# Kernel optimization log

Measured on AMD Instinct MI355X. Metric: run time of the kernel, lower is better.

The kernel has to match this reference:

```python
import jax, jax.numpy as jnp
import numpy as np

N_HEADS = 12


def setup_inputs() -> dict:
    key = jax.random.key(0)
    ks = jax.random.split(key, 5)
    B, T, D = 4, 2048, 768
    std = 1.0 / np.sqrt(D)
    return {
        "x": jax.random.normal(ks[0], (B, T, D), jnp.float32),
        "W_qkv": jax.random.normal(ks[1], (3 * D, D), jnp.float32) * std,
        "b_qkv": jax.random.normal(ks[2], (3 * D,), jnp.float32) * 0.02,
        "W_proj": jax.random.normal(ks[3], (D, D), jnp.float32) * std,
        "b_proj": jax.random.normal(ks[4], (D,), jnp.float32) * 0.02,
    }


def reference(x, W_qkv, b_qkv, W_proj, b_proj):
    # x: [B, T, D]; intended 3D path of the module (dropout = eval-mode identity)
    B, T, D = x.shape
    H = N_HEADS
    Dh = D // H
    scale = Dh ** -0.5
    qkv = x @ W_qkv.T + b_qkv                       # [B, T, 3D]
    qkv = qkv.reshape(B, T, 3, H, Dh)
    q = jnp.transpose(qkv[:, :, 0], (0, 2, 1, 3))    # [B, H, T, Dh]
    k = jnp.transpose(qkv[:, :, 1], (0, 2, 1, 3))
    v = jnp.transpose(qkv[:, :, 2], (0, 2, 1, 3))
    attn = jnp.einsum("bhqd,bhkd->bhqk", q, k) * scale  # [B, H, T, T]
    scores = jax.nn.softmax(attn, axis=-1)
    out = jnp.einsum("bhqk,bhkd->bhqd", scores, v)       # [B, H, T, Dh]
    out = jnp.transpose(out, (0, 2, 1, 3)).reshape(B, T, D)
    return out @ W_proj.T + b_proj
```

## Files before the change

kernel.cpp:

```cpp
#include <hip/hip_runtime.h>
#include <hip/hip_bf16.h>
#include <stdint.h>

typedef __bf16 bf16;
typedef __bf16 bf16x8 __attribute__((ext_vector_type(8)));
typedef __bf16 bf16x4 __attribute__((ext_vector_type(4)));
typedef short  s16x4  __attribute__((ext_vector_type(4)));
typedef short  s16x8  __attribute__((ext_vector_type(8)));
typedef float  f32x4  __attribute__((ext_vector_type(4)));

#define N_B 4
#define N_T 2048
#define N_D 768
#define N_H 12
#define N_DH 64
#define M_TOT (N_B * N_T)

__device__ __forceinline__ void async_copy16(const bf16* g, bf16* l) {
    __builtin_amdgcn_global_load_lds(
        (const __attribute__((address_space(1))) unsigned int*)g,
        (__attribute__((address_space(3))) unsigned int*)l,
        16, 0, 0);
}

__launch_bounds__(256)
__global__ void f2bf3(const float* __restrict__ a, bf16* __restrict__ oa, int na,
                      const float* __restrict__ b, bf16* __restrict__ ob, int nb,
                      const float* __restrict__ c, bf16* __restrict__ oc) {
    int i = (blockIdx.x * 256 + threadIdx.x) * 4;
    const float* src; bf16* dst;
    if (i < na)            { src = a; dst = oa; }
    else if (i < na + nb)  { src = b; dst = ob; i -= na; }
    else                   { src = c; dst = oc; i -= na + nb; }
    const float4 v = *(const float4*)(src + i);
    dst[i]     = (bf16)v.x;
    dst[i + 1] = (bf16)v.y;
    dst[i + 2] = (bf16)v.z;
    dst[i + 3] = (bf16)v.w;
}

#define GEMM_CORE(A_PTR, B_PTR, KDIM)                                          \
    __shared__ bf16 lsA[128 * 32];                                             \
    __shared__ bf16 lsB[128 * 32];                                             \
    const int m0 = blockIdx.x * 128;                                           \
    const int n0 = blockIdx.y * 128;                                           \
    const int t  = threadIdx.x;                                                \
    const int w  = t >> 6, l = t & 63;                                         \
    const int wm = w & 1, wn = w >> 1;                                         \
    const int lr = l & 15, lq = l >> 4;                                        \
    f32x4 acc[4][4] = {};                                                      \
    const bf16* Ab = (A_PTR) + (size_t)(m0 + (t >> 2)) * (KDIM) + (t & 3) * 8; \
    const bf16* Bb = (B_PTR) + (size_t)(n0 + (t >> 2)) * (KDIM) + (t & 3) * 8; \
    bf16* lA = lsA + t * 8;                                                    \
    bf16* lB = lsB + t * 8;                                                    \
    for (int k0 = 0; k0 < (KDIM); k0 += 32) {                                  \
        __syncthreads();                                                       \
        async_copy16(Ab + k0, lA);                                             \
        async_copy16(Ab + (size_t)64 * (KDIM) + k0, lA + 2048);                \
        async_copy16(Bb + k0, lB);                                             \
        async_copy16(Bb + (size_t)64 * (KDIM) + k0, lB + 2048);                \
        __syncthreads();                                                       \
        bf16x8 af[4], bfr[4];                                                  \
        for (int i = 0; i < 4; i++) {                                          \
            af[i]  = *(const bf16x8*)(lsA + (wm * 64 + i * 16 + lr) * 32 + lq * 8); \
            bfr[i] = *(const bf16x8*)(lsB + (wn * 64 + i * 16 + lr) * 32 + lq * 8); \
        }                                                                      \
        for (int i = 0; i < 4; i++)                                            \
            for (int j = 0; j < 4; j++)                                        \
                acc[i][j] = __builtin_amdgcn_mfma_f32_16x16x32_bf16(           \
                    af[i], bfr[j], acc[i][j], 0, 0, 0);                        \
    }

__launch_bounds__(256)
__global__ void gemm_qkv(const bf16* __restrict__ X, const bf16* __restrict__ W,
                         const float* __restrict__ bias,
                         bf16* __restrict__ Q, bf16* __restrict__ K,
                         bf16* __restrict__ Vt) {
    GEMM_CORE(X, W, 768)
    for (int i = 0; i < 4; i++) {
        const int rowb = m0 + wm * 64 + i * 16 + lq * 4;
        const int b_ = rowb >> 11, tt = rowb & 2047;
        for (int j = 0; j < 4; j++) {
            const int col   = n0 + wn * 64 + j * 16 + lr;
            const int which = col / 768;
            const int rem   = col - which * 768;
            const int h     = rem >> 6, d = rem & 63;
            const float bv  = bias[col];
            if (which == 2) {
                const int tile = tt >> 6, kl = tt & 63;
                const int kc = kl >> 4, r = kl & 15;
                const int idx = ((r >> 2) << 4) + (kc << 2);
                bf16x4 v4;
                for (int r2 = 0; r2 < 4; r2++) v4[r2] = (bf16)(acc[i][j][r2] + bv);
                *(bf16x4*)(Vt + ((size_t)((b_ * N_H + h) * 64 + d)) * 2048
                           + tile * 64 + idx) = v4;
            } else {
                bf16* dst = (which == 0) ? Q : K;
                const float sc = (which == 0) ? 0.18033688f : 1.0f;
                for (int r2 = 0; r2 < 4; r2++)
                    dst[(size_t)(((b_ * N_H + h) << 11) + tt + r2) * 64 + d] =
                        (bf16)((acc[i][j][r2] + bv) * sc);
            }
        }
    }
}

__launch_bounds__(256)
__global__ void gemm_proj(const bf16* __restrict__ O, const bf16* __restrict__ W,
                          const float* __restrict__ bias, float* __restrict__ out) {
    GEMM_CORE(O, W, 768)
    for (int i = 0; i < 4; i++) {
        const int rowb = m0 + wm * 64 + i * 16 + lq * 4;
        for (int j = 0; j < 4; j++) {
            const int col  = n0 + wn * 64 + j * 16 + lr;
            const float bv = bias[col];
            for (int r = 0; r < 4; r++)
                out[(size_t)(rowb + r) * 768 + col] = acc[i][j][r] + bv;
        }
    }
}

__launch_bounds__(512)
__global__ void attn(const bf16* __restrict__ Q, const bf16* __restrict__ K,
                     const bf16* __restrict__ Vt, bf16* __restrict__ O) {
    __shared__ bf16 lsK[2][64 * 64];
    __shared__ bf16 lsV[2][64 * 64];
    const int bid = blockIdx.x;
    const int xcd = bid & 7, slot = bid >> 3;
    const int bh  = xcd + 8 * (slot >> 4);
    const int qt  = slot & 15;
    const int t = threadIdx.x, w = t >> 6, l = t & 63;
    const int lr = l & 15, lq = l >> 4;
    const bf16* Qh  = Q  + (size_t)bh * N_T * 64;
    const bf16* Kh  = K  + (size_t)bh * N_T * 64;
    const bf16* Vth = Vt + (size_t)bh * 64 * N_T;
    const int q0 = qt * 128 + w * 16;

    const int sr = t >> 3;
    const int sp = t & 7;
    const int scn = sp ^ (sr & 7);

    bf16x8 qf[2];
    for (int ks = 0; ks < 2; ks++)
        qf[ks] = *(const bf16x8*)(Qh + (size_t)(q0 + lr) * 64 + ks * 32 + lq * 8);

    f32x4 oacc[4] = {};
    f32x4 lacc = {};
    const s16x4 ones = {0x3F80, 0x3F80, 0x3F80, 0x3F80};

    async_copy16(Kh  + (size_t)sr * 64 + scn * 8,   lsK[0] + t * 8);
    async_copy16(Vth + (size_t)sr * 2048 + scn * 8, lsV[0] + t * 8);

    for (int kt = 0; kt < 32; kt++) {
        const int cur = kt & 1;
        __syncthreads();

        if (kt < 31) {
            async_copy16(Kh  + (size_t)((kt + 1) * 64 + sr) * 64 + scn * 8,
                         lsK[cur ^ 1] + t * 8);
            async_copy16(Vth + (size_t)sr * 2048 + (kt + 1) * 64 + scn * 8,
                         lsV[cur ^ 1] + t * 8);
        }

        f32x4 sacc[4] = {};
        for (int ks = 0; ks < 2; ks++)
            for (int ki = 0; ki < 4; ki++) {
                const int row = ki * 16 + lr;
                bf16x8 kf = *(const bf16x8*)(lsK[cur] + row * 64 + ((ks * 4 + lq) ^ (lr & 7)) * 8);
                sacc[ki] = __builtin_amdgcn_mfma_f32_16x16x32_bf16(
                    kf, qf[ks], sacc[ki], 0, 0, 0);
            }

        s16x4 pbf[4];
        for (int ki = 0; ki < 4; ki++) {
            bf16x4 pb;
            for (int r = 0; r < 4; r++)
                pb[r] = (bf16)exp2f(sacc[ki][r]);
            pbf[ki] = __builtin_bit_cast(s16x4, pb);
        }

        for (int c = 0; c < 2; c++)
            for (int dj = 0; dj < 4; dj++) {
                const int row = dj * 16 + lr;
                const int unit = (2 * lq + c) ^ (lr & 7);
                s16x8 vv = *(const s16x8*)(lsV[cur] + row * 64 + unit * 8);
                s16x4 vlo = __builtin_shufflevector(vv, vv, 0, 1, 2, 3);
                s16x4 vhi = __builtin_shufflevector(vv, vv, 4, 5, 6, 7);
                oacc[dj] = __builtin_amdgcn_mfma_f32_16x16x16bf16_1k(
                    vlo, pbf[2 * c], oacc[dj], 0, 0, 0);
                oacc[dj] = __builtin_amdgcn_mfma_f32_16x16x16bf16_1k(
                    vhi, pbf[2 * c + 1], oacc[dj], 0, 0, 0);
            }
        for (int kc = 0; kc < 4; kc++)
            lacc = __builtin_amdgcn_mfma_f32_16x16x16bf16_1k(
                ones, pbf[kc], lacc, 0, 0, 0);
    }

    const int b = bh / N_H, h = bh - b * N_H;
    const float inv_l = 1.0f / lacc[0];
    const int tok = q0 + lr;
    bf16* Ob = O + ((size_t)b * N_T + tok) * N_D + h * 64;
    for (int dj = 0; dj < 4; dj++) {
        bf16x4 o4;
        for (int r = 0; r < 4; r++) o4[r] = (bf16)(oacc[dj][r] * inv_l);
        *(bf16x4*)(Ob + dj * 16 + lq * 4) = o4;
    }
}

extern "C" void kernel_launch(void* const* d_in, const int* in_sizes, int n_in,
                              void* d_out, int out_size, void* d_ws, size_t ws_size,
                              hipStream_t stream) {
    const float* x      = (const float*)d_in[0];
    const float* W_qkv  = (const float*)d_in[1];
    const float* b_qkv  = (const float*)d_in[2];
    const float* W_proj = (const float*)d_in[3];
    const float* b_proj = (const float*)d_in[4];
    float* out = (float*)d_out;

    char* ws = (char*)d_ws;
    const size_t n_x  = (size_t)M_TOT * N_D;
    const size_t n_wq = (size_t)3 * N_D * N_D;
    const size_t n_wp = (size_t)N_D * N_D;
    const size_t sz_qkv = (size_t)N_B * N_H * N_T * N_DH * sizeof(bf16);

    bf16* xb  = (bf16*)(ws);                 ws += n_x * sizeof(bf16);
    bf16* Wqb = (bf16*)(ws);                 ws += n_wq * sizeof(bf16);
    bf16* Wpb = (bf16*)(ws);                 ws += n_wp * sizeof(bf16);
    bf16* Qb  = (bf16*)(ws);                 ws += sz_qkv;
    bf16* Kb  = (bf16*)(ws);                 ws += sz_qkv;
    bf16* Vtb = (bf16*)(ws);                 ws += sz_qkv;
    bf16* Ob  = (bf16*)(ws);

    dim3 blk(256);
    f2bf3<<<dim3((int)((n_x + n_wq + n_wp) / 1024)), blk, 0, stream>>>(
        x, xb, (int)n_x, W_qkv, Wqb, (int)n_wq, W_proj, Wpb);

    gemm_qkv<<<dim3(M_TOT / 128, 2304 / 128), blk, 0, stream>>>(xb, Wqb, b_qkv, Qb, Kb, Vtb);
    attn<<<dim3(768), dim3(512), 0, stream>>>(Qb, Kb, Vtb, Ob);
    gemm_proj<<<dim3(M_TOT / 128, 768 / 128), blk, 0, stream>>>(Ob, Wpb, b_proj, out);
}
```

Baseline: 232.3 us.

## Split attention key tile across wave pairs with two query subtiles per wave

Each wave now handles 32 queries (two 16-row subtiles) and half of each 64-key tile, and the two key halves are combined at the end through shared memory. Every K and V fragment read from LDS is reused for two query subtiles, which halves LDS read traffic per MFMA. In exchange the kernel needs more accumulator registers and adds an LDS reduction pass with two extra block barriers at the end.

```diff
diff --git a/kernel.cpp b/kernel.cpp
--- a/kernel.cpp
+++ b/kernel.cpp
@@ -123,33 +123,36 @@
 __launch_bounds__(512)
 __global__ void attn(const bf16* __restrict__ Q, const bf16* __restrict__ K,
                      const bf16* __restrict__ Vt, bf16* __restrict__ O) {
-    __shared__ bf16 lsK[2][64 * 64];
-    __shared__ bf16 lsV[2][64 * 64];
+    __shared__ bf16 lsKV[4][64 * 64];
+    __shared__ float lsl[128];
     const int bid = blockIdx.x;
     const int xcd = bid & 7, slot = bid >> 3;
     const int bh  = xcd + 8 * (slot >> 4);
     const int qt  = slot & 15;
     const int t = threadIdx.x, w = t >> 6, l = t & 63;
     const int lr = l & 15, lq = l >> 4;
+    const int g  = w & 3;
+    const int kh = w >> 2;
     const bf16* Qh  = Q  + (size_t)bh * N_T * 64;
     const bf16* Kh  = K  + (size_t)bh * N_T * 64;
     const bf16* Vth = Vt + (size_t)bh * 64 * N_T;
-    const int q0 = qt * 128 + w * 16;
+    const int q0 = qt * 128 + g * 32;
 
     const int sr = t >> 3;
     const int sp = t & 7;
     const int scn = sp ^ (sr & 7);
 
-    bf16x8 qf[2];
-    for (int ks = 0; ks < 2; ks++)
-        qf[ks] = *(const bf16x8*)(Qh + (size_t)(q0 + lr) * 64 + ks * 32 + lq * 8);
-
-    f32x4 oacc[4] = {};
-    f32x4 lacc = {};
+    bf16x8 qf[2][2];
+    for (int s = 0; s < 2; s++)
+        for (int ks = 0; ks < 2; ks++)
+            qf[s][ks] = *(const bf16x8*)(Qh + (size_t)(q0 + s * 16 + lr) * 64 + ks * 32 + lq * 8);
+
+    f32x4 oacc[2][4] = {};
+    f32x4 lacc[2] = {};
     const s16x4 ones = {0x3F80, 0x3F80, 0x3F80, 0x3F80};
 
-    async_copy16(Kh  + (size_t)sr * 64 + scn * 8,   lsK[0] + t * 8);
-    async_copy16(Vth + (size_t)sr * 2048 + scn * 8, lsV[0] + t * 8);
+    async_copy16(Kh  + (size_t)sr * 64 + scn * 8,   lsKV[0] + t * 8);
+    async_copy16(Vth + (size_t)sr * 2048 + scn * 8, lsKV[2] + t * 8);
 
     for (int kt = 0; kt < 32; kt++) {
         const int cur = kt & 1;
@@ -157,53 +160,73 @@
 
         if (kt < 31) {
             async_copy16(Kh  + (size_t)((kt + 1) * 64 + sr) * 64 + scn * 8,
-                         lsK[cur ^ 1] + t * 8);
+                         lsKV[cur ^ 1] + t * 8);
             async_copy16(Vth + (size_t)sr * 2048 + (kt + 1) * 64 + scn * 8,
-                         lsV[cur ^ 1] + t * 8);
-        }
-
-        f32x4 sacc[4] = {};
+                         lsKV[2 + (cur ^ 1)] + t * 8);
+        }
+
+        f32x4 sacc[2][2] = {};
         for (int ks = 0; ks < 2; ks++)
-            for (int ki = 0; ki < 4; ki++) {
-                const int row = ki * 16 + lr;
-                bf16x8 kf = *(const bf16x8*)(lsK[cur] + row * 64 + ((ks * 4 + lq) ^ (lr & 7)) * 8);
-                sacc[ki] = __builtin_amdgcn_mfma_f32_16x16x32_bf16(
-                    kf, qf[ks], sacc[ki], 0, 0, 0);
-            }
-
-        s16x4 pbf[4];
-        for (int ki = 0; ki < 4; ki++) {
-            bf16x4 pb;
-            for (int r = 0; r < 4; r++)
-                pb[r] = (bf16)exp2f(sacc[ki][r]);
-            pbf[ki] = __builtin_bit_cast(s16x4, pb);
-        }
-
-        for (int c = 0; c < 2; c++)
+            for (int ki = 0; ki < 2; ki++) {
+                const int row = kh * 32 + ki * 16 + lr;
+                bf16x8 kf = *(const bf16x8*)(lsKV[cur] + row * 64 + ((ks * 4 + lq) ^ (lr & 7)) * 8);
+                for (int s = 0; s < 2; s++)
+                    sacc[s][ki] = __builtin_amdgcn_mfma_f32_16x16x32_bf16(
+                        kf, qf[s][ks], sacc[s][ki], 0, 0, 0);
+            }
+
+        s16x4 pbf[2][2];
+        for (int s = 0; s < 2; s++)
+            for (int ki = 0; ki < 2; ki++) {
+                bf16x4 pb;
+                for (int r = 0; r < 4; r++)
+                    pb[r] = (bf16)exp2f(sacc[s][ki][r]);
+                pbf[s][ki] = __builtin_bit_cast(s16x4, pb);
+            }
+
+        for (int dj = 0; dj < 4; dj++) {
+            const int row = dj * 16 + lr;
+            const int unit = (2 * lq + kh) ^ (lr & 7);
+            s16x8 vv = *(const s16x8*)(lsKV[2 + cur] + row * 64 + unit * 8);
+            s16x4 vlo = __builtin_shufflevector(vv, vv, 0, 1, 2, 3);
+            s16x4 vhi = __builtin_shufflevector(vv, vv, 4, 5, 6, 7);
+            for (int s = 0; s < 2; s++) {
+                oacc[s][dj] = __builtin_amdgcn_mfma_f32_16x16x16bf16_1k(
+                    vlo, pbf[s][0], oacc[s][dj], 0, 0, 0);
+                oacc[s][dj] = __builtin_amdgcn_mfma_f32_16x16x16bf16_1k(
+                    vhi, pbf[s][1], oacc[s][dj], 0, 0, 0);
+            }
+        }
+        for (int s = 0; s < 2; s++) {
+            lacc[s] = __builtin_amdgcn_mfma_f32_16x16x16bf16_1k(ones, pbf[s][0], lacc[s], 0, 0, 0);
+            lacc[s] = __builtin_amdgcn_mfma_f32_16x16x16bf16_1k(ones, pbf[s][1], lacc[s], 0, 0, 0);
+        }
+    }
+
+    __syncthreads();
+    float* ex = (float*)lsKV;
+    if (kh) {
+        for (int s = 0; s < 2; s++) {
+            for (int dj = 0; dj < 4; dj++)
+                *(f32x4*)(ex + ((g * 2 + s) * 16 + lr) * 64 + dj * 16 + lq * 4) = oacc[s][dj];
+            lsl[(g * 2 + s) * 16 + lr] = lacc[s][0];
+        }
+    }
+    __syncthreads();
+    if (!kh) {
+        const int b = bh / N_H, h = bh - b * N_H;
+        for (int s = 0; s < 2; s++) {
+            for (int dj = 0; dj < 4; dj++)
+                oacc[s][dj] += *(const f32x4*)(ex + ((g * 2 + s) * 16 + lr) * 64 + dj * 16 + lq * 4);
+            const float inv_l = 1.0f / (lacc[s][0] + lsl[(g * 2 + s) * 16 + lr]);
+            const int tok = q0 + s * 16 + lr;
+            bf16* Ob = O + ((size_t)b * N_T + tok) * N_D + h * 64;
             for (int dj = 0; dj < 4; dj++) {
-                const int row = dj * 16 + lr;
-                const int unit = (2 * lq + c) ^ (lr & 7);
-                s16x8 vv = *(const s16x8*)(lsV[cur] + row * 64 + unit * 8);
-                s16x4 vlo = __builtin_shufflevector(vv, vv, 0, 1, 2, 3);
-                s16x4 vhi = __builtin_shufflevector(vv, vv, 4, 5, 6, 7);
-                oacc[dj] = __builtin_amdgcn_mfma_f32_16x16x16bf16_1k(
-                    vlo, pbf[2 * c], oacc[dj], 0, 0, 0);
-                oacc[dj] = __builtin_amdgcn_mfma_f32_16x16x16bf16_1k(
-                    vhi, pbf[2 * c + 1], oacc[dj], 0, 0, 0);
-            }
-        for (int kc = 0; kc < 4; kc++)
-            lacc = __builtin_amdgcn_mfma_f32_16x16x16bf16_1k(
-                ones, pbf[kc], lacc, 0, 0, 0);
-    }
-
-    const int b = bh / N_H, h = bh - b * N_H;
-    const float inv_l = 1.0f / lacc[0];
-    const int tok = q0 + lr;
-    bf16* Ob = O + ((size_t)b * N_T + tok) * N_D + h * 64;
-    for (int dj = 0; dj < 4; dj++) {
-        bf16x4 o4;
-        for (int r = 0; r < 4; r++) o4[r] = (bf16)(oacc[dj][r] * inv_l);
-        *(bf16x4*)(Ob + dj * 16 + lq * 4) = o4;
+                bf16x4 o4;
+                for (int r = 0; r < 4; r++) o4[r] = (bf16)(oacc[s][dj][r] * inv_l);
+                *(bf16x4*)(Ob + dj * 16 + lq * 4) = o4;
+            }
+        }
     }
 }
 
```

New measurement: 240.3 us. +3.5%, slower.

## Software-pipeline attention loop: overlap QK^T of next tile with softmax/PV of previous

Applied to the files above, without the earlier changes.

Restructures the attention inner loop so that the QK^T MFMAs for key tile i are issued in the same iteration as the exp and PV MFMAs for tile i-1. This needs a prologue that computes the first tile's scores and an epilogue for the last tile. V gets a triple LDS buffer because the previous V tile must stay live one iteration longer. The aim is to let exp/VALU work overlap with matrix-core work. In exchange it raises register pressure, adds LDS usage, and adds a launch-bounds occupancy hint (min 6 blocks).

```diff
diff --git a/kernel.cpp b/kernel.cpp
--- a/kernel.cpp
+++ b/kernel.cpp
@@ -120,11 +120,11 @@
     }
 }
 
-__launch_bounds__(512)
+__launch_bounds__(512, 6)
 __global__ void attn(const bf16* __restrict__ Q, const bf16* __restrict__ K,
                      const bf16* __restrict__ Vt, bf16* __restrict__ O) {
     __shared__ bf16 lsK[2][64 * 64];
-    __shared__ bf16 lsV[2][64 * 64];
+    __shared__ bf16 lsV[3][64 * 64];
     const int bid = blockIdx.x;
     const int xcd = bid & 7, slot = bid >> 3;
     const int bh  = xcd + 8 * (slot >> 4);
@@ -150,40 +150,81 @@
 
     async_copy16(Kh  + (size_t)sr * 64 + scn * 8,   lsK[0] + t * 8);
     async_copy16(Vth + (size_t)sr * 2048 + scn * 8, lsV[0] + t * 8);
-
-    for (int kt = 0; kt < 32; kt++) {
-        const int cur = kt & 1;
+    __syncthreads();
+    async_copy16(Kh  + (size_t)(64 + sr) * 64 + scn * 8, lsK[1] + t * 8);
+    async_copy16(Vth + (size_t)sr * 2048 + 64 + scn * 8, lsV[1] + t * 8);
+
+    f32x4 sprev[4] = {};
+    for (int ks = 0; ks < 2; ks++)
+        for (int ki = 0; ki < 4; ki++) {
+            bf16x8 kf = *(const bf16x8*)(lsK[0] + (ki * 16 + lr) * 64
+                                         + ((ks * 4 + lq) ^ (lr & 7)) * 8);
+            sprev[ki] = __builtin_amdgcn_mfma_f32_16x16x32_bf16(
+                kf, qf[ks], sprev[ki], 0, 0, 0);
+        }
+
+    int vprev = 0, vcur = 1, vnext = 2;
+
+    for (int i = 1; i < 32; i++) {
         __syncthreads();
 
-        if (kt < 31) {
-            async_copy16(Kh  + (size_t)((kt + 1) * 64 + sr) * 64 + scn * 8,
-                         lsK[cur ^ 1] + t * 8);
-            async_copy16(Vth + (size_t)sr * 2048 + (kt + 1) * 64 + scn * 8,
-                         lsV[cur ^ 1] + t * 8);
-        }
-
-        f32x4 sacc[4] = {};
+        if (i < 31) {
+            async_copy16(Kh  + (size_t)((i + 1) * 64 + sr) * 64 + scn * 8,
+                         lsK[(i + 1) & 1] + t * 8);
+            async_copy16(Vth + (size_t)sr * 2048 + (i + 1) * 64 + scn * 8,
+                         lsV[vnext] + t * 8);
+        }
+
+        f32x4 snew[4] = {};
         for (int ks = 0; ks < 2; ks++)
             for (int ki = 0; ki < 4; ki++) {
-                const int row = ki * 16 + lr;
-                bf16x8 kf = *(const bf16x8*)(lsK[cur] + row * 64 + ((ks * 4 + lq) ^ (lr & 7)) * 8);
-                sacc[ki] = __builtin_amdgcn_mfma_f32_16x16x32_bf16(
-                    kf, qf[ks], sacc[ki], 0, 0, 0);
+                bf16x8 kf = *(const bf16x8*)(lsK[i & 1] + (ki * 16 + lr) * 64
+                                             + ((ks * 4 + lq) ^ (lr & 7)) * 8);
+                snew[ki] = __builtin_amdgcn_mfma_f32_16x16x32_bf16(
+                    kf, qf[ks], snew[ki], 0, 0, 0);
             }
 
         s16x4 pbf[4];
         for (int ki = 0; ki < 4; ki++) {
             bf16x4 pb;
             for (int r = 0; r < 4; r++)
-                pb[r] = (bf16)exp2f(sacc[ki][r]);
+                pb[r] = (bf16)exp2f(sprev[ki][r]);
             pbf[ki] = __builtin_bit_cast(s16x4, pb);
         }
 
+        const bf16* vb = lsV[vprev];
         for (int c = 0; c < 2; c++)
             for (int dj = 0; dj < 4; dj++) {
-                const int row = dj * 16 + lr;
                 const int unit = (2 * lq + c) ^ (lr & 7);
-                s16x8 vv = *(const s16x8*)(lsV[cur] + row * 64 + unit * 8);
+                s16x8 vv = *(const s16x8*)(vb + (dj * 16 + lr) * 64 + unit * 8);
+                s16x4 vlo = __builtin_shufflevector(vv, vv, 0, 1, 2, 3);
+                s16x4 vhi = __builtin_shufflevector(vv, vv, 4, 5, 6, 7);
+                oacc[dj] = __builtin_amdgcn_mfma_f32_16x16x16bf16_1k(
+                    vlo, pbf[2 * c], oacc[dj], 0, 0, 0);
+                oacc[dj] = __builtin_amdgcn_mfma_f32_16x16x16bf16_1k(
+                    vhi, pbf[2 * c + 1], oacc[dj], 0, 0, 0);
+            }
+        for (int kc = 0; kc < 4; kc++)
+            lacc = __builtin_amdgcn_mfma_f32_16x16x16bf16_1k(
+                ones, pbf[kc], lacc, 0, 0, 0);
+
+        for (int ki = 0; ki < 4; ki++) sprev[ki] = snew[ki];
+        const int tmp = vprev; vprev = vcur; vcur = vnext; vnext = tmp;
+    }
+
+    {
+        s16x4 pbf[4];
+        for (int ki = 0; ki < 4; ki++) {
+            bf16x4 pb;
+            for (int r = 0; r < 4; r++)
+                pb[r] = (bf16)exp2f(sprev[ki][r]);
+            pbf[ki] = __builtin_bit_cast(s16x4, pb);
+        }
+        const bf16* vb = lsV[vprev];
+        for (int c = 0; c < 2; c++)
+            for (int dj = 0; dj < 4; dj++) {
+                const int unit = (2 * lq + c) ^ (lr & 7);
+                s16x8 vv = *(const s16x8*)(vb + (dj * 16 + lr) * 64 + unit * 8);
                 s16x4 vlo = __builtin_shufflevector(vv, vv, 0, 1, 2, 3);
                 s16x4 vhi = __builtin_shufflevector(vv, vv, 4, 5, 6, 7);
                 oacc[dj] = __builtin_amdgcn_mfma_f32_16x16x16bf16_1k(
```

New measurement: 234.5 us. Within noise of the previous version (+0.9%).
